# Kernel tuning notes

Measured on AMD Instinct MI355X. Metric: run time of the kernel, lower is better.

The kernel has to match this reference:

```python
import jax, jax.numpy as jnp
import numpy as np

D_MODEL = 256
N_HEADS = 4
WINDOW = 8
DECAY = 0.9
STEP_SIZE = 0.5


def _linear(x, w, b):
    # torch nn.Linear: y = x @ w.T + b, w: [out, in]
    return jnp.einsum('...i,oi->...o', x, w) + b


def _layernorm(x, scale, bias, eps=1e-5):
    mu = jnp.mean(x, axis=-1, keepdims=True)
    var = jnp.var(x, axis=-1, keepdims=True)
    return (x - mu) * jax.lax.rsqrt(var + eps) * scale + bias


def _ema(x, decay):
    # ema[t] = decay*ema[t-1] + (1-decay)*x[t], ema[-1]=0
    # (exactly the causal conv with weights (1-d)*d^i from the torch code)
    def step(c, xt):
        c = decay * c + (1.0 - decay) * xt
        return c, c
    _, ys = jax.lax.scan(step, jnp.zeros_like(x[:, 0]), jnp.swapaxes(x, 0, 1))
    return jnp.swapaxes(ys, 0, 1)


def setup_inputs() -> dict:
    key = jax.random.key(0)
    ks = iter(jax.random.split(key, 40))
    B, T, D = 8, 1024, D_MODEL
    s = 0.02
    inp = {
        'parallel_repr': jax.random.normal(next(ks), (B, T, D), jnp.float32),
        'sequential_state': jax.random.normal(next(ks), (B, D), jnp.float32),
        'trajectory_summary': jax.random.normal(next(ks), (B, D), jnp.float32),
        # MultiheadAttention params
        'in_proj_w': jax.random.normal(next(ks), (3 * D, D), jnp.float32) * s,
        'in_proj_b': jnp.zeros((3 * D,), jnp.float32),
        'out_proj_w': jax.random.normal(next(ks), (D, D), jnp.float32) * s,
        'out_proj_b': jnp.zeros((D,), jnp.float32),
        # depthwise causal conv (local history)
        'conv_w': jax.random.normal(next(ks), (D, 1, WINDOW), jnp.float32) * s,
        'conv_b': jnp.zeros((D,), jnp.float32),
        # parallel_to_sequential / sequential_to_parallel
        'p2s_w': jax.random.normal(next(ks), (D, D), jnp.float32) * s,
        'p2s_b': jnp.zeros((D,), jnp.float32),
        's2p_w': jax.random.normal(next(ks), (D, D), jnp.float32) * s,
        's2p_b': jnp.zeros((D,), jnp.float32),
        # transition MLP: 3D -> 2D -> D
        'trans_w1': jax.random.normal(next(ks), (2 * D, 3 * D), jnp.float32) * s,
        'trans_b1': jnp.zeros((2 * D,), jnp.float32),
        'trans_w2': jax.random.normal(next(ks), (D, 2 * D), jnp.float32) * s,
        'trans_b2': jnp.zeros((D,), jnp.float32),
        # FFN: D -> 4D -> D
        'ffn_w1': jax.random.normal(next(ks), (4 * D, D), jnp.float32) * s,
        'ffn_b1': jnp.zeros((4 * D,), jnp.float32),
        'ffn_w2': jax.random.normal(next(ks), (D, 4 * D), jnp.float32) * s,
        'ffn_b2': jnp.zeros((D,), jnp.float32),
        # LayerNorms
        'ln1_s': jnp.ones((D,), jnp.float32), 'ln1_b': jnp.zeros((D,), jnp.float32),
        'ln2_s': jnp.ones((D,), jnp.float32), 'ln2_b': jnp.zeros((D,), jnp.float32),
        'ln3_s': jnp.ones((D,), jnp.float32), 'ln3_b': jnp.zeros((D,), jnp.float32),
        'ln4_s': jnp.ones((D,), jnp.float32), 'ln4_b': jnp.zeros((D,), jnp.float32),
    }
    return inp


def _forward(parallel_repr, sequential_state,
             in_proj_w, in_proj_b, out_proj_w, out_proj_b,
             conv_w, conv_b, p2s_w, p2s_b, s2p_w, s2p_b,
             trans_w1, trans_b1, trans_w2, trans_b2,
             ffn_w1, ffn_b1, ffn_w2, ffn_b2,
             ln1_s, ln1_b, ln2_s, ln2_b, ln3_s, ln3_b, ln4_s, ln4_b):
    B, T, D = parallel_repr.shape
    H, hd = N_HEADS, D // N_HEADS

    # --- causal self-attention (nn.MultiheadAttention, batch_first) ---
    qkv = _linear(parallel_repr, in_proj_w, in_proj_b)
    q, k, v = jnp.split(qkv, 3, axis=-1)
    q = q.reshape(B, T, H, hd)
    k = k.reshape(B, T, H, hd)
    v = v.reshape(B, T, H, hd)
    scores = jnp.einsum('bqhd,bkhd->bhqk', q, k) / jnp.sqrt(jnp.asarray(hd, q.dtype))
    causal = jnp.triu(jnp.ones((T, T), bool), 1)
    scores = jnp.where(causal, jnp.finfo(scores.dtype).min, scores)
    attn = jax.nn.softmax(scores, axis=-1)
    attn_out = jnp.einsum('bhqk,bkhd->bqhd', attn, v).reshape(B, T, D)
    attn_out = _linear(attn_out, out_proj_w, out_proj_b)
    x = _layernorm(parallel_repr + attn_out, ln1_s, ln1_b)

    # --- depthwise causal conv (local history) ---
    xt = jnp.swapaxes(x, 1, 2)  # [B, D, T]
    xt_pad = jnp.pad(xt, ((0, 0), (0, 0), (WINDOW - 1, 0)))
    local = jax.lax.conv_general_dilated(
        xt_pad, conv_w, window_strides=(1,), padding='VALID',
        dimension_numbers=('NCH', 'OIH', 'NCH'), feature_group_count=D)
    local_history = jnp.swapaxes(local + conv_b[None, :, None], 1, 2)  # [B, T, D]

    # --- global EMA summary ---
    global_summary = _ema(x, DECAY)

    # --- transition deltas + cumsum state integration ---
    parallel_guidance = _linear(x, p2s_w, p2s_b)
    combined = jnp.concatenate([x + 0.3 * parallel_guidance, local_history, global_summary], axis=-1)
    h = jax.nn.gelu(_linear(combined, trans_w1, trans_b1), approximate=False)
    deltas = _linear(h, trans_w2, trans_b2)
    states = sequential_state[:, None, :] + jnp.cumsum(deltas, axis=1) * STEP_SIZE
    states = _layernorm(states, ln3_s, ln3_b)

    # --- FFN with sequential guidance ---
    seq_guidance = _linear(states, s2p_w, s2p_b)
    f = jax.nn.gelu(_linear(x + 0.3 * seq_guidance, ffn_w1, ffn_b1), approximate=False)
    ffn_out = _linear(f, ffn_w2, ffn_b2)
    x = _layernorm(x + ffn_out, ln2_s, ln2_b)

    final_sequential_state = _layernorm(states[:, -1, :], ln4_s, ln4_b)
    final_trajectory_summary = global_summary[:, -1, :]
    return x, final_sequential_state, final_trajectory_summary


def reference(parallel_repr, sequential_state, trajectory_summary,
              in_proj_w, in_proj_b, out_proj_w, out_proj_b,
              conv_w, conv_b, p2s_w, p2s_b, s2p_w, s2p_b,
              trans_w1, trans_b1, trans_w2, trans_b2,
              ffn_w1, ffn_b1, ffn_w2, ffn_b2,
              ln1_s, ln1_b, ln2_s, ln2_b, ln3_s, ln3_b, ln4_s, ln4_b):
    # trajectory_summary is accepted by the torch forward but never used.
    return _forward(parallel_repr, sequential_state,
                    in_proj_w, in_proj_b, out_proj_w, out_proj_b,
                    conv_w, conv_b, p2s_w, p2s_b, s2p_w, s2p_b,
                    trans_w1, trans_b1, trans_w2, trans_b2,
                    ffn_w1, ffn_b1, ffn_w2, ffn_b2,
                    ln1_s, ln1_b, ln2_s, ln2_b, ln3_s, ln3_b, ln4_s, ln4_b)
```

## Files before the change

kernel.cpp:

```cpp
#include <hip/hip_runtime.h>
#include <math.h>

typedef unsigned short u16;
typedef __attribute__((ext_vector_type(8))) short bf16x8;
typedef __attribute__((ext_vector_type(4))) float f32x4;

#define D_MODEL 256
#define T_SZ 1024
constexpr size_t S_ELT = (size_t)8192 * 256;
constexpr size_t MB = 1024 * 1024;

constexpr size_t OFF_QKV = 0;
constexpr size_t OFF_ATTN = 12 * MB;
constexpr size_t OFF_F = 0;
constexpr size_t OFF_X = 16 * MB;
constexpr size_t OFF_COMB = 24 * MB;
constexpr size_t OFF_FB = 36 * MB;
constexpr size_t OFF_H = 44 * MB;
constexpr size_t OFF_XBF = 48 * MB;
constexpr size_t OFF_WB = 52 * MB;
constexpr size_t OFF_SCR1 = 55 * MB;
constexpr size_t OFF_SCR2 = 55 * MB + 262144;

constexpr int WB_INPROJ = 0;
constexpr int WB_OUTPROJ = 196608;
constexpr int WB_P2S = 262144;
constexpr int WB_S2P = 327680;
constexpr int WB_T1 = 393216;
constexpr int WB_T2 = 786432;
constexpr int WB_F1 = 917504;
constexpr int WB_F2 = 1179648;
constexpr int WB_TOTAL = 1441792;
constexpr int PR_TOTAL = 2097152;

__device__ __forceinline__ u16 f2bf(float f) {
  unsigned int u = __float_as_uint(f);
  u += 0x7fff + ((u >> 16) & 1);
  return (u16)(u >> 16);
}
__device__ __forceinline__ float bf2f(u16 s) {
  return __uint_as_float(((unsigned int)s) << 16);
}

__device__ __forceinline__ void glds16(const u16* g, u16* l) {
  __builtin_amdgcn_global_load_lds(
      (const __attribute__((address_space(1))) void*)g,
      (__attribute__((address_space(3))) void*)l, 16, 0, 0);
}

__global__ __launch_bounds__(256)
void wconv_kernel(const float* w0, const float* w1, const float* w2,
                  const float* w3, const float* w4, const float* w5,
                  const float* w6, const float* w7, const float* pr,
                  u16* __restrict__ wb, u16* __restrict__ prb) {
  const int idx4 = (blockIdx.x * 256 + threadIdx.x) * 4;
  if (idx4 < WB_TOTAL) {
    const int offs[9] = {WB_INPROJ, WB_OUTPROJ, WB_P2S,  WB_S2P, WB_T1,
                         WB_T2,     WB_F1,      WB_F2,   WB_TOTAL};
    const float* srcs[8] = {w0, w1, w2, w3, w4, w5, w6, w7};
    int seg = 0;
    while (idx4 >= offs[seg + 1]) ++seg;
    float4 v = *(const float4*)(srcs[seg] + (idx4 - offs[seg]));
    unsigned int lo = (unsigned int)f2bf(v.x) | ((unsigned int)f2bf(v.y) << 16);
    unsigned int hi = (unsigned int)f2bf(v.z) | ((unsigned int)f2bf(v.w) << 16);
    *(uint2*)(wb + idx4) = make_uint2(lo, hi);
  } else {
    const int i4 = idx4 - WB_TOTAL;
    if (i4 < PR_TOTAL) {
      float4 v = *(const float4*)(pr + i4);
      unsigned int lo = (unsigned int)f2bf(v.x) | ((unsigned int)f2bf(v.y) << 16);
      unsigned int hi = (unsigned int)f2bf(v.z) | ((unsigned int)f2bf(v.w) << 16);
      *(uint2*)(prb + i4) = make_uint2(lo, hi);
    }
  }
}

enum { EPI_NONE = 0, EPI_GELU = 1, EPI_ADDSCALE = 2 };

template <int EPI, int BM, int BN, bool OUTBF, bool VSPLIT>
__global__ __launch_bounds__(256, 4)
void mgemm(const u16* __restrict__ A, int lda,
           const u16* __restrict__ Wb, int K, const float* __restrict__ bias,
           void* __restrict__ Cv, int ldc, int col_off,
           const float* __restrict__ addsrc, u16* __restrict__ vt) {
  __shared__ u16 As[BM * 64];
  __shared__ u16 Bs[BN * 64];
  const int tid = threadIdx.x;
  const int w = tid >> 6, lane = tid & 63;
  const int ln = lane & 15, quad = lane >> 4;
  const int m0 = blockIdx.x * BM;
  const int n0 = blockIdx.y * BN;
  constexpr int MT = (BM == 128) ? 2 : 1;
  const int wm = w * (MT * 16);
  constexpr int wn = 0;
  constexpr int APW = BM / 64;
  constexpr int BPW = BN / 64;

  f32x4 acc[MT][4] = {};

  const int grow = lane >> 2;
  const int gk8 = (lane & 3) * 8;

  for (int k0 = 0; k0 < K; k0 += 64) {
#pragma unroll
    for (int s = 0; s < 2; ++s) {
#pragma unroll
      for (int p = 0; p < APW; ++p) {
        const int g = w * APW + p;
        glds16(A + (size_t)(m0 + g * 16 + grow) * lda + k0 + s * 32 + gk8,
               As + s * BM * 32 + g * 512);
      }
#pragma unroll
      for (int p = 0; p < BPW; ++p) {
        const int g = w * BPW + p;
        glds16(Wb + (size_t)(n0 + g * 16 + grow) * K + k0 + s * 32 + gk8,
               Bs + s * BN * 32 + g * 512);
      }
    }
    __syncthreads();
#pragma unroll
    for (int s = 0; s < 2; ++s) {
      const u16* abase = As + s * BM * 32 + (wm >> 4) * 512 + ln * 32 + quad * 8;
      const u16* bbase = Bs + s * BN * 32 + ln * 32 + quad * 8;
      bf16x8 af[MT], bv[4];
#pragma unroll
      for (int i = 0; i < MT; ++i) af[i] = *(const bf16x8*)(abase + i * 512);
#pragma unroll
      for (int j = 0; j < 4; ++j) bv[j] = *(const bf16x8*)(bbase + j * 512);
#pragma unroll
      for (int i = 0; i < MT; ++i)
#pragma unroll
        for (int j = 0; j < 4; ++j)
          acc[i][j] = __builtin_amdgcn_mfma_f32_16x16x32_bf16(af[i], bv[j],
                                                              acc[i][j], 0, 0, 0);
    }
    __syncthreads();
  }

#pragma unroll
  for (int i = 0; i < MT; ++i)
#pragma unroll
    for (int j = 0; j < 4; ++j) {
      const int col = n0 + wn + j * 16 + ln;
      const float bsv = bias[col];
      const int row0 = m0 + wm + i * 16 + quad * 4;
      float vals[4];
#pragma unroll
      for (int r = 0; r < 4; ++r) {
        float v = acc[i][j][r] + bsv;
        if (EPI == EPI_GELU) v = 0.5f * v * (1.0f + erff(v * 0.70710678f));
        if (EPI == EPI_ADDSCALE)
          v = addsrc[(size_t)(row0 + r) * 256 + col] + 0.3f * v;
        vals[r] = v;
      }
      if (VSPLIT && col >= 512) {
        ushort4 pk;
        pk.x = f2bf(vals[0]); pk.y = f2bf(vals[1]);
        pk.z = f2bf(vals[2]); pk.w = f2bf(vals[3]);
        *(ushort4*)(vt + (size_t)((row0 >> 10) * 256 + (col - 512)) * T_SZ +
                    (row0 & 1023)) = pk;
      } else if (OUTBF) {
#pragma unroll
        for (int r = 0; r < 4; ++r)
          ((u16*)Cv)[(size_t)(row0 + r) * ldc + col_off + col] = f2bf(vals[r]);
      } else {
#pragma unroll
        for (int r = 0; r < 4; ++r)
          ((float*)Cv)[(size_t)(row0 + r) * ldc + col_off + col] = vals[r];
      }
    }
}

template <bool WRITE_BF>
__global__ __launch_bounds__(256, 4)
void mgemm_ln16(const u16* __restrict__ A, const u16* __restrict__ Wb, int K,
                const float* __restrict__ bias, const float* __restrict__ addsrc,
                const float* __restrict__ g, const float* __restrict__ bb,
                float* __restrict__ outf, u16* __restrict__ outbf) {
  __shared__ u16 As[2 * 512];
  __shared__ u16 Bs[2 * 8192];
  __shared__ float tS1[4][16], tS2[4][16];
  const int tid = threadIdx.x;
  const int w = tid >> 6, lane = tid & 63;
  const int ln = lane & 15, quad = lane >> 4;
  const int m0 = blockIdx.x * 16;
  const int grow = lane >> 2;
  const int gk8 = (lane & 3) * 8;

  f32x4 acc[4] = {};

  for (int k0 = 0; k0 < K; k0 += 64) {
    if (w < 2)
      glds16(A + (size_t)(m0 + grow) * K + k0 + w * 32 + gk8, As + w * 512);
#pragma unroll
    for (int p = 0; p < 8; ++p) {
      const int idx = w * 8 + p;
      const int s = idx >> 4, gg = idx & 15;
      glds16(Wb + (size_t)(gg * 16 + grow) * K + k0 + s * 32 + gk8,
             Bs + s * 8192 + gg * 512);
    }
    __syncthreads();
#pragma unroll
    for (int s = 0; s < 2; ++s) {
      const bf16x8 af = *(const bf16x8*)(As + s * 512 + ln * 32 + quad * 8);
      const u16* bbase = Bs + s * 8192 + (w * 4) * 512 + ln * 32 + quad * 8;
#pragma unroll
      for (int j = 0; j < 4; ++j) {
        bf16x8 bv = *(const bf16x8*)(bbase + j * 512);
        acc[j] = __builtin_amdgcn_mfma_f32_16x16x32_bf16(af, bv, acc[j], 0, 0, 0);
      }
    }
    __syncthreads();
  }

  const int row0 = m0 + quad * 4;
  float s1[4] = {}, s2[4] = {};
#pragma unroll
  for (int j = 0; j < 4; ++j) {
    const int col = w * 64 + j * 16 + ln;
    const float bsv = bias[col];
#pragma unroll
    for (int r = 0; r < 4; ++r) {
      float v = acc[j][r] + bsv + addsrc[(size_t)(row0 + r) * 256 + col];
      acc[j][r] = v;
      s1[r] += v;
      s2[r] += v * v;
    }
  }
#pragma unroll
  for (int r = 0; r < 4; ++r) {
#pragma unroll
    for (int o = 8; o > 0; o >>= 1) {
      s1[r] += __shfl_xor(s1[r], o);
      s2[r] += __shfl_xor(s2[r], o);
    }
  }
  if (ln == 0) {
#pragma unroll
    for (int r = 0; r < 4; ++r) {
      tS1[w][quad * 4 + r] = s1[r];
      tS2[w][quad * 4 + r] = s2[r];
    }
  }
  __syncthreads();
  float mean[4], inv[4];
#pragma unroll
  for (int r = 0; r < 4; ++r) {
    const int qr = quad * 4 + r;
    const float S1 = tS1[0][qr] + tS1[1][qr] + tS1[2][qr] + tS1[3][qr];
    const float S2 = tS2[0][qr] + tS2[1][qr] + tS2[2][qr] + tS2[3][qr];
    mean[r] = S1 * (1.f / 256.f);
    const float var = S2 * (1.f / 256.f) - mean[r] * mean[r];
    inv[r] = rsqrtf(var + 1e-5f);
  }
#pragma unroll
  for (int j = 0; j < 4; ++j) {
    const int col = w * 64 + j * 16 + ln;
    const float gc = g[col], bc = bb[col];
#pragma unroll
    for (int r = 0; r < 4; ++r) {
      const float y = (acc[j][r] - mean[r]) * inv[r] * gc + bc;
      outf[(size_t)(row0 + r) * 256 + col] = y;
      if (WRITE_BF) outbf[(size_t)(row0 + r) * 256 + col] = f2bf(y);
    }
  }
}

__global__ __launch_bounds__(256)
void attn_flash(const u16* __restrict__ qkv, const u16* __restrict__ vt,
                u16* __restrict__ outp) {
  __shared__ u16 Ps[4][16][72];
  const int tid = threadIdx.x;
  const int w = tid >> 6, lane = tid & 63;
  const int ln = lane & 15, quad = lane >> 4, kq8 = quad * 8;
  const int wu = blockIdx.x * 4 + w;
  const int bh = wu >> 6, s = wu & 63;
  const int qt = (s & 1) ? (63 - (s >> 1)) : (s >> 1);
  const int q0 = qt * 16;
  const int b = bh >> 2, h = bh & 3;
  const u16* base = qkv + (size_t)b * T_SZ * 768;
  const u16* vbase = vt + (size_t)bh * 64 * T_SZ;

  bf16x8 qf[2];
#pragma unroll
  for (int ks = 0; ks < 2; ++ks)
    qf[ks] = *(const bf16x8*)(base + (size_t)(q0 + ln) * 768 + h * 64 +
                              ks * 32 + kq8);
  const short ob = (short)0x3F80;
  const bf16x8 ones = {ob, ob, ob, ob, ob, ob, ob, ob};

  f32x4 O[4] = {};
  f32x4 l_acc = {};
  const int ntiles = (qt >> 2) + 1;
  for (int jt = 0; jt < ntiles; ++jt) {
    const int c0 = jt * 64;
    f32x4 sv[4] = {};
#pragma unroll
    for (int ks = 0; ks < 2; ++ks)
#pragma unroll
      for (int j = 0; j < 4; ++j) {
        bf16x8 kf = *(const bf16x8*)(base + (size_t)(c0 + j * 16 + ln) * 768 +
                                     256 + h * 64 + ks * 32 + kq8);
        sv[j] = __builtin_amdgcn_mfma_f32_16x16x32_bf16(qf[ks], kf, sv[j], 0, 0, 0);
      }
    const bool need_mask = (c0 + 63 > q0);
#pragma unroll
    for (int j = 0; j < 4; ++j)
#pragma unroll
      for (int r = 0; r < 4; ++r) {
        float p = __expf(sv[j][r] * 0.125f);
        if (need_mask && (c0 + j * 16 + ln > q0 + quad * 4 + r)) p = 0.f;
        Ps[w][quad * 4 + r][j * 16 + ln] = f2bf(p);
      }
#pragma unroll
    for (int ks = 0; ks < 2; ++ks) {
      bf16x8 pf = *(const bf16x8*)&Ps[w][ln][ks * 32 + kq8];
      l_acc = __builtin_amdgcn_mfma_f32_16x16x32_bf16(pf, ones, l_acc, 0, 0, 0);
#pragma unroll
      for (int j = 0; j < 4; ++j) {
        bf16x8 vf = *(const bf16x8*)(vbase + (size_t)(j * 16 + ln) * T_SZ +
                                     c0 + ks * 32 + kq8);
        O[j] = __builtin_amdgcn_mfma_f32_16x16x32_bf16(pf, vf, O[j], 0, 0, 0);
      }
    }
  }
  u16* op = outp + (size_t)b * T_SZ * 256;
#pragma unroll
  for (int r = 0; r < 4; ++r) {
    const float inv = 1.f / l_acc[r];
#pragma unroll
    for (int j = 0; j < 4; ++j)
      op[(size_t)(q0 + quad * 4 + r) * 256 + h * 64 + j * 16 + ln] =
          f2bf(O[j][r] * inv);
  }
}

__device__ __forceinline__ void block_reduce_2(float& a, float& q, float* tmp) {
#pragma unroll
  for (int o = 32; o > 0; o >>= 1) {
    a += __shfl_down(a, o);
    q += __shfl_down(q, o);
  }
  const int lane = threadIdx.x & 63, wid = threadIdx.x >> 6;
  if (lane == 0) { tmp[wid] = a; tmp[4 + wid] = q; }
  __syncthreads();
  a = tmp[0] + tmp[1] + tmp[2] + tmp[3];
  q = tmp[4] + tmp[5] + tmp[6] + tmp[7];
  __syncthreads();
}

__device__ __forceinline__ float ln_finish(float v, float s1, float s2,
                                           float g, float bb) {
  float mean = s1 * (1.f / 256.f);
  float var = s2 * (1.f / 256.f) - mean * mean;
  return (v - mean) * rsqrtf(var + 1e-5f) * g + bb;
}

__global__ __launch_bounds__(256)
void emaconv_kernel(const float* __restrict__ x, const float* __restrict__ cw,
                    const float* __restrict__ cb, u16* __restrict__ comb,
                    float* __restrict__ scr) {
  const int bc = blockIdx.x;
  const int b = bc >> 5, ch = bc & 31;
  const int d = threadIdx.x;
  const int t0 = ch * 32;
  float wreg[8];
#pragma unroll
  for (int j = 0; j < 8; ++j) wreg[j] = cw[d * 8 + j];
  const float bias = cb[d];
  float xw[8];
#pragma unroll
  for (int j = 0; j < 7; ++j) {
    const int ts = t0 - 7 + j;
    xw[j] = (ts >= 0) ? x[(size_t)(b * T_SZ + ts) * 256 + d] : 0.f;
  }
  float c = 0.f;
#pragma unroll
  for (int tl = 0; tl < 32; ++tl) {
    const size_t row = (size_t)(b * T_SZ + t0 + tl);
    xw[7] = x[row * 256 + d];
    float conv = bias;
#pragma unroll
    for (int j = 0; j < 8; ++j) conv = fmaf(xw[j], wreg[j], conv);
    c = 0.9f * c + 0.1f * xw[7];
    comb[row * 768 + 256 + d] = f2bf(conv);
    comb[row * 768 + 512 + d] = f2bf(c);
#pragma unroll
    for (int j = 0; j < 7; ++j) xw[j] = xw[j + 1];
  }
  scr[(size_t)bc * 256 + d] = c;
}

__global__ __launch_bounds__(256)
void ema_b_kernel(float* __restrict__ scr) {
  const int b = blockIdx.x, d = threadIdx.x;
  const float q32 = 0.03433683820292512f;
  float carry = 0.f;
  for (int ch = 0; ch < 32; ++ch) {
    const size_t idx = (size_t)(b * 32 + ch) * 256 + d;
    float e = scr[idx];
    scr[idx] = carry;
    carry = e + q32 * carry;
  }
}

__global__ __launch_bounds__(256)
void ema_c_kernel(u16* __restrict__ comb, const float* __restrict__ scr,
                  float* __restrict__ fts) {
  const int row = blockIdx.x;
  const int b = row >> 10, t = row & 1023;
  const int d = threadIdx.x;
  const int ch = t >> 5, tl = t & 31;
  float carry = scr[(size_t)(b * 32 + ch) * 256 + d];
  float l = bf2f(comb[(size_t)row * 768 + 512 + d]);
  float y = fmaf(__powf(0.9f, (float)(tl + 1)), carry, l);
  comb[(size_t)row * 768 + 512 + d] = f2bf(y);
  if (t == 1023) fts[b * 256 + d] = y;
}

__global__ __launch_bounds__(256)
void cs_a_kernel(float* __restrict__ deltas, float* __restrict__ scr) {
  const int bc = blockIdx.x;
  const int b = bc >> 5, ch = bc & 31;
  const int d = threadIdx.x;
  const int t0 = ch * 32;
  float c = 0.f;
  for (int tl = 0; tl < 32; ++tl) {
    const size_t idx = (size_t)(b * T_SZ + t0 + tl) * 256 + d;
    c += deltas[idx];
    deltas[idx] = c;
  }
  scr[(size_t)bc * 256 + d] = c;
}

__global__ __launch_bounds__(256)
void cs_b_kernel(float* __restrict__ scr) {
  const int b = blockIdx.x, d = threadIdx.x;
  float carry = 0.f;
  for (int ch = 0; ch < 32; ++ch) {
    const size_t idx = (size_t)(b * 32 + ch) * 256 + d;
    float e = scr[idx];
    scr[idx] = carry;
    carry += e;
  }
}

__global__ __launch_bounds__(256)
void ln3_states_kernel(const float* __restrict__ deltas, const float* __restrict__ scr,
                       const float* __restrict__ seq, const float* __restrict__ g3,
                       const float* __restrict__ b3, const float* __restrict__ g4,
                       const float* __restrict__ b4, u16* __restrict__ st,
                       float* __restrict__ fss) {
  __shared__ float tmp[8];
  const int row = blockIdx.x;
  const int b = row >> 10, t = row & 1023;
  const int d = threadIdx.x;
  float v = seq[b * 256 + d] +
            0.5f * (deltas[(size_t)row * 256 + d] +
                    scr[(size_t)(b * 32 + (t >> 5)) * 256 + d]);
  float a = v, q = v * v;
  block_reduce_2(a, q, tmp);
  const float y = ln_finish(v, a, q, g3[d], b3[d]);
  st[(size_t)row * 256 + d] = f2bf(y);
  if (t == 1023) {
    float a2 = y, q2 = y * y;
    block_reduce_2(a2, q2, tmp);
    fss[b * 256 + d] = ln_finish(y, a2, q2, g4[d], b4[d]);
  }
}

extern "C" void kernel_launch(void* const* d_in, const int* in_sizes, int n_in,
                              void* d_out, int out_size, void* d_ws,
                              size_t ws_size, hipStream_t stream) {
  (void)in_sizes; (void)n_in; (void)out_size; (void)ws_size;
  const float* parallel_repr = (const float*)d_in[0];
  const float* sequential_state = (const float*)d_in[1];
  const float* in_proj_b = (const float*)d_in[4];
  const float* out_proj_b = (const float*)d_in[6];
  const float* conv_w = (const float*)d_in[7];
  const float* conv_b = (const float*)d_in[8];
  const float* p2s_b = (const float*)d_in[10];
  const float* s2p_b = (const float*)d_in[12];
  const float* trans_b1 = (const float*)d_in[14];
  const float* trans_b2 = (const float*)d_in[16];
  const float* ffn_b1 = (const float*)d_in[18];
  const float* ffn_b2 = (const float*)d_in[20];
  const float* ln1_s = (const float*)d_in[21];
  const float* ln1_b = (const float*)d_in[22];
  const float* ln2_s = (const float*)d_in[23];
  const float* ln2_b = (const float*)d_in[24];
  const float* ln3_s = (const float*)d_in[25];
  const float* ln3_b = (const float*)d_in[26];
  const float* ln4_s = (const float*)d_in[27];
  const float* ln4_b = (const float*)d_in[28];

  char* ws = (char*)d_ws;
  u16* qkv_bf = (u16*)(ws + OFF_QKV);
  u16* attn_bf = (u16*)(ws + OFF_ATTN);
  u16* states_bf = (u16*)(ws + OFF_ATTN);
  u16* f_bf = (u16*)(ws + OFF_F);
  float* x = (float*)(ws + OFF_X);
  u16* comb = (u16*)(ws + OFF_COMB);
  u16* pr_bf = (u16*)(ws + OFF_COMB);
  u16* ffn_in = (u16*)(ws + OFF_COMB);
  float* fbuf = (float*)(ws + OFF_FB);
  u16* vt = (u16*)(ws + OFF_H);
  u16* h_bf = (u16*)(ws + OFF_H);
  u16* x_bf = (u16*)(ws + OFF_XBF);
  u16* wb = (u16*)(ws + OFF_WB);
  float* scr1 = (float*)(ws + OFF_SCR1);
  float* scr2 = (float*)(ws + OFF_SCR2);
  float* out = (float*)d_out;
  float* out_fss = out + S_ELT;
  float* out_fts = out + S_ELT + 2048;

  const dim3 blk(256);

  wconv_kernel<<<3456, blk, 0, stream>>>(
      (const float*)d_in[3], (const float*)d_in[5], (const float*)d_in[9],
      (const float*)d_in[11], (const float*)d_in[13], (const float*)d_in[15],
      (const float*)d_in[17], (const float*)d_in[19], parallel_repr, wb, pr_bf);
  mgemm<EPI_NONE, 128, 64, true, true><<<dim3(64, 12), blk, 0, stream>>>(
      pr_bf, 256, wb + WB_INPROJ, 256, in_proj_b, qkv_bf, 768, 0, nullptr, vt);
  attn_flash<<<512, blk, 0, stream>>>(qkv_bf, vt, attn_bf);
  mgemm_ln16<true><<<512, blk, 0, stream>>>(
      attn_bf, wb + WB_OUTPROJ, 256, out_proj_b, parallel_repr, ln1_s, ln1_b,
      x, x_bf);
  emaconv_kernel<<<256, blk, 0, stream>>>(x, conv_w, conv_b, comb, scr1);
  ema_b_kernel<<<8, blk, 0, stream>>>(scr1);
  ema_c_kernel<<<8192, blk, 0, stream>>>(comb, scr1, out_fts);
  mgemm<EPI_ADDSCALE, 64, 64, true, false><<<dim3(128, 4), blk, 0, stream>>>(
      x_bf, 256, wb + WB_P2S, 256, p2s_b, comb, 768, 0, x, nullptr);
  mgemm<EPI_GELU, 128, 64, true, false><<<dim3(64, 8), blk, 0, stream>>>(
      comb, 768, wb + WB_T1, 768, trans_b1, h_bf, 512, 0, nullptr, nullptr);
  mgemm<EPI_NONE, 64, 64, false, false><<<dim3(128, 4), blk, 0, stream>>>(
      h_bf, 512, wb + WB_T2, 512, trans_b2, fbuf, 256, 0, nullptr, nullptr);
  cs_a_kernel<<<256, blk, 0, stream>>>(fbuf, scr2);
  cs_b_kernel<<<8, blk, 0, stream>>>(scr2);
  ln3_states_kernel<<<8192, blk, 0, stream>>>(fbuf, scr2, sequential_state,
                                              ln3_s, ln3_b, ln4_s, ln4_b,
                                              states_bf, out_fss);
  mgemm<EPI_ADDSCALE, 64, 64, true, false><<<dim3(128, 4), blk, 0, stream>>>(
      states_bf, 256, wb + WB_S2P, 256, s2p_b, ffn_in, 256, 0, x, nullptr);
  mgemm<EPI_GELU, 128, 64, true, false><<<dim3(64, 16), blk, 0, stream>>>(
      ffn_in, 256, wb + WB_F1, 256, ffn_b1, f_bf, 1024, 0, nullptr, nullptr);
  mgemm_ln16<false><<<512, blk, 0, stream>>>(
      f_bf, wb + WB_F2, 1024, ffn_b2, x, ln2_s, ln2_b, out, nullptr);
}
```

Baseline: 260.3 us.

## Fuse EMA carry fixup with p2s GEMM and drop scan-carry kernels

Removes the serial ema_b and cs_b carry-propagation kernels. Each chunk now recomputes its prefix carry from the per-chunk partials. The EMA correction and the p2s GEMM are merged into one launch, with extra blocks handling the EMA fixup, and the cumulative-sum carry is recomputed inside ln3_states. This cuts three kernel launches and their serial 8-block phases, at the cost of redundant O(chunks) reads per thread and a hand-written GEMM path replacing the templated mgemm.

```diff
diff --git a/kernel.cpp b/kernel.cpp
--- a/kernel.cpp
+++ b/kernel.cpp
@@ -391,31 +391,76 @@
   scr[(size_t)bc * 256 + d] = c;
 }
 
-__global__ __launch_bounds__(256)
-void ema_b_kernel(float* __restrict__ scr) {
-  const int b = blockIdx.x, d = threadIdx.x;
-  const float q32 = 0.03433683820292512f;
-  float carry = 0.f;
-  for (int ch = 0; ch < 32; ++ch) {
-    const size_t idx = (size_t)(b * 32 + ch) * 256 + d;
-    float e = scr[idx];
-    scr[idx] = carry;
-    carry = e + q32 * carry;
-  }
-}
-
-__global__ __launch_bounds__(256)
-void ema_c_kernel(u16* __restrict__ comb, const float* __restrict__ scr,
-                  float* __restrict__ fts) {
-  const int row = blockIdx.x;
-  const int b = row >> 10, t = row & 1023;
-  const int d = threadIdx.x;
-  const int ch = t >> 5, tl = t & 31;
-  float carry = scr[(size_t)(b * 32 + ch) * 256 + d];
-  float l = bf2f(comb[(size_t)row * 768 + 512 + d]);
-  float y = fmaf(__powf(0.9f, (float)(tl + 1)), carry, l);
-  comb[(size_t)row * 768 + 512 + d] = f2bf(y);
-  if (t == 1023) fts[b * 256 + d] = y;
+__global__ __launch_bounds__(256, 4)
+void emac_p2s(const u16* __restrict__ xbf, const u16* __restrict__ wbp,
+              const float* __restrict__ bias, const float* __restrict__ x,
+              u16* __restrict__ comb, const float* __restrict__ scr1,
+              float* __restrict__ fts) {
+  __shared__ u16 As[64 * 64];
+  __shared__ u16 Bs[64 * 64];
+  const int rb = blockIdx.x;
+  const int tid = threadIdx.x;
+  if (rb < 512) {
+    const int w = tid >> 6, lane = tid & 63;
+    const int ln = lane & 15, quad = lane >> 4;
+    const int m0 = (rb & 127) * 64;
+    const int n0 = (rb >> 7) * 64;
+    const int grow = lane >> 2, gk8 = (lane & 3) * 8;
+    f32x4 acc[4] = {};
+    for (int k0 = 0; k0 < 256; k0 += 64) {
+#pragma unroll
+      for (int s = 0; s < 2; ++s) {
+        glds16(xbf + (size_t)(m0 + w * 16 + grow) * 256 + k0 + s * 32 + gk8,
+               As + s * 2048 + w * 512);
+        glds16(wbp + (size_t)(n0 + w * 16 + grow) * 256 + k0 + s * 32 + gk8,
+               Bs + s * 2048 + w * 512);
+      }
+      __syncthreads();
+#pragma unroll
+      for (int s = 0; s < 2; ++s) {
+        const u16* abase = As + s * 2048 + w * 512 + ln * 32 + quad * 8;
+        const u16* bbase = Bs + s * 2048 + ln * 32 + quad * 8;
+        bf16x8 af = *(const bf16x8*)abase;
+#pragma unroll
+        for (int j = 0; j < 4; ++j) {
+          bf16x8 bv = *(const bf16x8*)(bbase + j * 512);
+          acc[j] = __builtin_amdgcn_mfma_f32_16x16x32_bf16(af, bv, acc[j], 0, 0, 0);
+        }
+      }
+      __syncthreads();
+    }
+    const int row0 = m0 + w * 16 + quad * 4;
+#pragma unroll
+    for (int j = 0; j < 4; ++j) {
+      const int col = n0 + j * 16 + ln;
+      const float bsv = bias[col];
+#pragma unroll
+      for (int r = 0; r < 4; ++r) {
+        float v = x[(size_t)(row0 + r) * 256 + col] + 0.3f * (acc[j][r] + bsv);
+        comb[(size_t)(row0 + r) * 768 + col] = f2bf(v);
+      }
+    }
+  } else {
+    const int bc = rb - 512;
+    const int b = bc >> 5, ch = bc & 31;
+    const int d = tid;
+    const float q32 = 0.03433683820292512f;
+    float carry = 0.f;
+    for (int j = 0; j < ch; ++j)
+      carry = scr1[(size_t)(b * 32 + j) * 256 + d] + q32 * carry;
+    const int t0 = ch * 32;
+    float pw = 0.9f;
+    float y = 0.f;
+#pragma unroll
+    for (int tl = 0; tl < 32; ++tl) {
+      const size_t row = (size_t)(b * T_SZ + t0 + tl);
+      const float l = bf2f(comb[row * 768 + 512 + d]);
+      y = fmaf(pw, carry, l);
+      comb[row * 768 + 512 + d] = f2bf(y);
+      pw *= 0.9f;
+    }
+    if (ch == 31) fts[b * 256 + d] = y;
+  }
 }
 
 __global__ __launch_bounds__(256)
@@ -434,18 +479,6 @@
 }
 
 __global__ __launch_bounds__(256)
-void cs_b_kernel(float* __restrict__ scr) {
-  const int b = blockIdx.x, d = threadIdx.x;
-  float carry = 0.f;
-  for (int ch = 0; ch < 32; ++ch) {
-    const size_t idx = (size_t)(b * 32 + ch) * 256 + d;
-    float e = scr[idx];
-    scr[idx] = carry;
-    carry += e;
-  }
-}
-
-__global__ __launch_bounds__(256)
 void ln3_states_kernel(const float* __restrict__ deltas, const float* __restrict__ scr,
                        const float* __restrict__ seq, const float* __restrict__ g3,
                        const float* __restrict__ b3, const float* __restrict__ g4,
@@ -455,9 +488,12 @@
   const int row = blockIdx.x;
   const int b = row >> 10, t = row & 1023;
   const int d = threadIdx.x;
+  const int ch = t >> 5;
+  float carry = 0.f;
+  for (int j = 0; j < ch; ++j)
+    carry += scr[(size_t)(b * 32 + j) * 256 + d];
   float v = seq[b * 256 + d] +
-            0.5f * (deltas[(size_t)row * 256 + d] +
-                    scr[(size_t)(b * 32 + (t >> 5)) * 256 + d]);
+            0.5f * (deltas[(size_t)row * 256 + d] + carry);
   float a = v, q = v * v;
   block_reduce_2(a, q, tmp);
   const float y = ln_finish(v, a, q, g3[d], b3[d]);
@@ -527,16 +563,13 @@
       attn_bf, wb + WB_OUTPROJ, 256, out_proj_b, parallel_repr, ln1_s, ln1_b,
       x, x_bf);
   emaconv_kernel<<<256, blk, 0, stream>>>(x, conv_w, conv_b, comb, scr1);
-  ema_b_kernel<<<8, blk, 0, stream>>>(scr1);
-  ema_c_kernel<<<8192, blk, 0, stream>>>(comb, scr1, out_fts);
-  mgemm<EPI_ADDSCALE, 64, 64, true, false><<<dim3(128, 4), blk, 0, stream>>>(
-      x_bf, 256, wb + WB_P2S, 256, p2s_b, comb, 768, 0, x, nullptr);
+  emac_p2s<<<768, blk, 0, stream>>>(x_bf, wb + WB_P2S, p2s_b, x, comb, scr1,
+                                    out_fts);
   mgemm<EPI_GELU, 128, 64, true, false><<<dim3(64, 8), blk, 0, stream>>>(
       comb, 768, wb + WB_T1, 768, trans_b1, h_bf, 512, 0, nullptr, nullptr);
   mgemm<EPI_NONE, 64, 64, false, false><<<dim3(128, 4), blk, 0, stream>>>(
       h_bf, 512, wb + WB_T2, 512, trans_b2, fbuf, 256, 0, nullptr, nullptr);
   cs_a_kernel<<<256, blk, 0, stream>>>(fbuf, scr2);
-  cs_b_kernel<<<8, blk, 0, stream>>>(scr2);
   ln3_states_kernel<<<8192, blk, 0, stream>>>(fbuf, scr2, sequential_state,
                                               ln3_s, ln3_b, ln4_s, ln4_b,
                                               states_bf, out_fss);
```

Measured after the change: 275.1 us. +5.7%, slower.

## Fold p2s projection into transition MLP first-layer weights and prioritize attention MFMAs

Applied to the files above, without the earlier changes.

The p2s linear feeding the first 256 columns of the transition input (x + 0.3*p2s(x)) is folded algebraically into trans_w1: a new per-call kernel computes W1' = W1 + 0.3*W1·P2S and an adjusted bias. The LN1 GEMM now writes its bf16 output directly into the concat buffer, so the separate p2s GEMM launch is removed. It also adds s_setprio around the MFMA blocks in flash attention to favour matrix-issue waves. The fold kernel is a scalar fp32 loop run every call, and it changes rounding because the folded weight is quantized to bf16 once.

```diff
diff --git a/kernel.cpp b/kernel.cpp
--- a/kernel.cpp
+++ b/kernel.cpp
@@ -21,6 +21,7 @@
 constexpr size_t OFF_WB = 52 * MB;
 constexpr size_t OFF_SCR1 = 55 * MB;
 constexpr size_t OFF_SCR2 = 55 * MB + 262144;
+constexpr size_t OFF_B1E = 55 * MB + 524288;
 
 constexpr int WB_INPROJ = 0;
 constexpr int WB_OUTPROJ = 196608;
@@ -75,6 +76,38 @@
   }
 }
 
+__global__ __launch_bounds__(256)
+void wfold_kernel(const float* __restrict__ t1, const float* __restrict__ p2s,
+                  const float* __restrict__ t1b, const float* __restrict__ p2sb,
+                  u16* __restrict__ wt1, float* __restrict__ b1e) {
+  __shared__ float trow[8][256];
+  const int o0 = blockIdx.x * 8;
+  const int k = threadIdx.x;
+#pragma unroll
+  for (int r = 0; r < 8; ++r)
+    trow[r][k] = t1[(size_t)(o0 + r) * 768 + k];
+  __syncthreads();
+  float acc[8] = {};
+  float bacc[8] = {};
+  for (int i = 0; i < 256; ++i) {
+    const float pv = p2s[(size_t)i * 256 + k];
+    const float pbv = p2sb[i];
+#pragma unroll
+    for (int r = 0; r < 8; ++r) {
+      acc[r] = fmaf(trow[r][i], pv, acc[r]);
+      bacc[r] = fmaf(trow[r][i], pbv, bacc[r]);
+    }
+  }
+#pragma unroll
+  for (int r = 0; r < 8; ++r)
+    wt1[(size_t)(o0 + r) * 768 + k] = f2bf(trow[r][k] + 0.3f * acc[r]);
+  if (k == 0) {
+#pragma unroll
+    for (int r = 0; r < 8; ++r)
+      b1e[o0 + r] = t1b[o0 + r] + 0.3f * bacc[r];
+  }
+}
+
 enum { EPI_NONE = 0, EPI_GELU = 1, EPI_ADDSCALE = 2 };
 
 template <int EPI, int BM, int BN, bool OUTBF, bool VSPLIT>
@@ -176,7 +209,7 @@
 void mgemm_ln16(const u16* __restrict__ A, const u16* __restrict__ Wb, int K,
                 const float* __restrict__ bias, const float* __restrict__ addsrc,
                 const float* __restrict__ g, const float* __restrict__ bb,
-                float* __restrict__ outf, u16* __restrict__ outbf) {
+                float* __restrict__ outf, u16* __restrict__ outbf, int bfldc) {
   __shared__ u16 As[2 * 512];
   __shared__ u16 Bs[2 * 8192];
   __shared__ float tS1[4][16], tS2[4][16];
@@ -261,7 +294,7 @@
     for (int r = 0; r < 4; ++r) {
       const float y = (acc[j][r] - mean[r]) * inv[r] * gc + bc;
       outf[(size_t)(row0 + r) * 256 + col] = y;
-      if (WRITE_BF) outbf[(size_t)(row0 + r) * 256 + col] = f2bf(y);
+      if (WRITE_BF) outbf[(size_t)(row0 + r) * bfldc + col] = f2bf(y);
     }
   }
 }
@@ -295,6 +328,7 @@
   for (int jt = 0; jt < ntiles; ++jt) {
     const int c0 = jt * 64;
     f32x4 sv[4] = {};
+    __builtin_amdgcn_s_setprio(1);
 #pragma unroll
     for (int ks = 0; ks < 2; ++ks)
 #pragma unroll
@@ -303,6 +337,7 @@
                                      256 + h * 64 + ks * 32 + kq8);
         sv[j] = __builtin_amdgcn_mfma_f32_16x16x32_bf16(qf[ks], kf, sv[j], 0, 0, 0);
       }
+    __builtin_amdgcn_s_setprio(0);
     const bool need_mask = (c0 + 63 > q0);
 #pragma unroll
     for (int j = 0; j < 4; ++j)
@@ -312,6 +347,7 @@
         if (need_mask && (c0 + j * 16 + ln > q0 + quad * 4 + r)) p = 0.f;
         Ps[w][quad * 4 + r][j * 16 + ln] = f2bf(p);
       }
+    __builtin_amdgcn_s_setprio(1);
 #pragma unroll
     for (int ks = 0; ks < 2; ++ks) {
       bf16x8 pf = *(const bf16x8*)&Ps[w][ln][ks * 32 + kq8];
@@ -323,6 +359,7 @@
         O[j] = __builtin_amdgcn_mfma_f32_16x16x32_bf16(pf, vf, O[j], 0, 0, 0);
       }
     }
+    __builtin_amdgcn_s_setprio(0);
   }
   u16* op = outp + (size_t)b * T_SZ * 256;
 #pragma unroll
@@ -479,8 +516,10 @@
   const float* out_proj_b = (const float*)d_in[6];
   const float* conv_w = (const float*)d_in[7];
   const float* conv_b = (const float*)d_in[8];
+  const float* p2s_w_f = (const float*)d_in[9];
   const float* p2s_b = (const float*)d_in[10];
   const float* s2p_b = (const float*)d_in[12];
+  const float* trans_w1_f = (const float*)d_in[13];
   const float* trans_b1 = (const float*)d_in[14];
   const float* trans_b2 = (const float*)d_in[16];
   const float* ffn_b1 = (const float*)d_in[18];
@@ -502,14 +541,14 @@
   float* x = (float*)(ws + OFF_X);
   u16* comb = (u16*)(ws + OFF_COMB);
   u16* pr_bf = (u16*)(ws + OFF_COMB);
-  u16* ffn_in = (u16*)(ws + OFF_COMB);
   float* fbuf = (float*)(ws + OFF_FB);
   u16* vt = (u16*)(ws + OFF_H);
   u16* h_bf = (u16*)(ws + OFF_H);
-  u16* x_bf = (u16*)(ws + OFF_XBF);
+  u16* ffn_in = (u16*)(ws + OFF_XBF);
   u16* wb = (u16*)(ws + OFF_WB);
   float* scr1 = (float*)(ws + OFF_SCR1);
   float* scr2 = (float*)(ws + OFF_SCR2);
+  float* b1e = (float*)(ws + OFF_B1E);
   float* out = (float*)d_out;
   float* out_fss = out + S_ELT;
   float* out_fts = out + S_ELT + 2048;
@@ -520,19 +559,19 @@
       (const float*)d_in[3], (const float*)d_in[5], (const float*)d_in[9],
       (const float*)d_in[11], (const float*)d_in[13], (const float*)d_in[15],
       (const float*)d_in[17], (const float*)d_in[19], parallel_repr, wb, pr_bf);
+  wfold_kernel<<<64, blk, 0, stream>>>(trans_w1_f, p2s_w_f, trans_b1, p2s_b,
+                                       wb + WB_T1, b1e);
   mgemm<EPI_NONE, 128, 64, true, true><<<dim3(64, 12), blk, 0, stream>>>(
       pr_bf, 256, wb + WB_INPROJ, 256, in_proj_b, qkv_bf, 768, 0, nullptr, vt);
   attn_flash<<<512, blk, 0, stream>>>(qkv_bf, vt, attn_bf);
   mgemm_ln16<true><<<512, blk, 0, stream>>>(
       attn_bf, wb + WB_OUTPROJ, 256, out_proj_b, parallel_repr, ln1_s, ln1_b,
-      x, x_bf);
+      x, comb, 768);
   emaconv_kernel<<<256, blk, 0, stream>>>(x, conv_w, conv_b, comb, scr1);
   ema_b_kernel<<<8, blk, 0, stream>>>(scr1);
   ema_c_kernel<<<8192, blk, 0, stream>>>(comb, scr1, out_fts);
-  mgemm<EPI_ADDSCALE, 64, 64, true, false><<<dim3(128, 4), blk, 0, stream>>>(
-      x_bf, 256, wb + WB_P2S, 256, p2s_b, comb, 768, 0, x, nullptr);
   mgemm<EPI_GELU, 128, 64, true, false><<<dim3(64, 8), blk, 0, stream>>>(
-      comb, 768, wb + WB_T1, 768, trans_b1, h_bf, 512, 0, nullptr, nullptr);
+      comb, 768, wb + WB_T1, 768, b1e, h_bf, 512, 0, nullptr, nullptr);
   mgemm<EPI_NONE, 64, 64, false, false><<<dim3(128, 4), blk, 0, stream>>>(
       h_bf, 512, wb + WB_T2, 512, trans_b2, fbuf, 256, 0, nullptr, nullptr);
   cs_a_kernel<<<256, blk, 0, stream>>>(fbuf, scr2);
@@ -545,5 +584,5 @@
   mgemm<EPI_GELU, 128, 64, true, false><<<dim3(64, 16), blk, 0, stream>>>(
       ffn_in, 256, wb + WB_F1, 256, ffn_b1, f_bf, 1024, 0, nullptr, nullptr);
   mgemm_ln16<false><<<512, blk, 0, stream>>>(
-      f_bf, wb + WB_F2, 1024, ffn_b2, x, ln2_s, ln2_b, out, nullptr);
-}
+      f_bf, wb + WB_F2, 1024, ffn_b2, x, ln2_s, ln2_b, out, nullptr, 256);
+}
```

After: 287.7 us. +10.5%, slower.
